# Optimization experiments

Hardware: AMD Instinct MI355X
Metric: run time of the kernel (lower is better)

## Reference

```python
import jax, jax.numpy as jnp
import numpy as np

TAU = 2.0   # membrane time constant
V_TH = 0.5  # firing threshold

@jax.custom_vjp
def spike_fn(v):
    return jnp.where(v > 0, 1.0, 0.0)

def _spike_fwd(v):
    return spike_fn(v), v

def _spike_bwd(v, g):
    # atan surrogate gradient (alpha=2): d s / d v = 1 / (1 + (pi*v)^2)
    sg = 1.0 / (1.0 + (jnp.pi * v) ** 2)
    return (g * sg,)

spike_fn.defvjp(_spike_fwd, _spike_bwd)


def setup_inputs() -> dict:
    key = jax.random.key(0)
    # [batch, neurons, time] -- time on axis 2, matching moveaxis(x, 2, 0)
    x = jax.random.normal(key, (32, 16384, 100), dtype=jnp.float32)
    return {"x": x}


def reference(x):
    x_seq = jnp.moveaxis(x, 2, 0)  # [T, B, N]
    decay = 1.0 - 1.0 / TAU

    def scan_fn(v, x_t):
        v = v * decay + x_t            # leaky integrate
        s = spike_fn(v - V_TH)         # fire
        v = v - s * V_TH               # soft reset
        return v, s

    v_init = jnp.zeros_like(x_seq[0])
    _, spikes = jax.lax.scan(scan_fn, v_init, x_seq)
    return jnp.moveaxis(spikes, 0, 2)  # [B, N, T]
```

## Files before the change

### kernel.cpp

```cpp
#include <hip/hip_runtime.h>
#include <stdint.h>


#define T_STEPS 100
#define T_VEC   25
#define ROWS    64
#define DECAY   0.5f
#define VTH     0.5f

typedef float vfloat4 __attribute__((ext_vector_type(4)));

__device__ __forceinline__ void gll16(const vfloat4* g, vfloat4* l) {
    __builtin_amdgcn_global_load_lds(
        (const __attribute__((address_space(1))) void*)g,
        (__attribute__((address_space(3))) void*)l,
        16, 0, 0);
}

__global__ __launch_bounds__(64) void lif_gll(const float* __restrict__ x,
                                              float* __restrict__ out,
                                              int n_rows) {
    __shared__ vfloat4 tile[ROWS * T_VEC];
    __shared__ uint4   bits[ROWS];

    const int lane = threadIdx.x;
    const int row0 = blockIdx.x * ROWS;
    const int gf0  = row0 * T_VEC;
    const int total_f4 = n_rows * T_VEC;

    const vfloat4* __restrict__ xb = reinterpret_cast<const vfloat4*>(x);

    unsigned int pk0 = 0, pk1 = 0, pk2 = 0, pk3 = 0;

    if (gf0 + ROWS * T_VEC <= total_f4) {
        #pragma unroll
        for (int k = 0; k < T_VEC; ++k)
            gll16(xb + (gf0 + k * 64 + lane), &tile[k * 64]);

        asm volatile("s_waitcnt vmcnt(0)" ::: "memory");
        __builtin_amdgcn_sched_barrier(0);

        float v = 0.0f;
        #pragma unroll
        for (int c = 0; c < T_VEC; ++c) {
            vfloat4 xs = tile[lane * T_VEC + c];
            #pragma unroll
            for (int k = 0; k < 4; ++k) {
                v = v * DECAY + xs[k];
                bool sp = (v - VTH > 0.0f);
                v -= sp ? VTH : 0.0f;
                unsigned int bit = sp ? 1u : 0u;
                const int b = c * 4 + k;
                if      (b < 32) pk0 |= bit << b;
                else if (b < 64) pk1 |= bit << (b - 32);
                else if (b < 96) pk2 |= bit << (b - 64);
                else             pk3 |= bit << (b - 96);
            }
        }
    } else {
        if (row0 + lane < n_rows) {
            const vfloat4* __restrict__ xr =
                xb + (long long)(row0 + lane) * T_VEC;
            float v = 0.0f;
            #pragma unroll
            for (int c = 0; c < T_VEC; ++c) {
                vfloat4 xs = xr[c];
                #pragma unroll
                for (int k = 0; k < 4; ++k) {
                    v = v * DECAY + xs[k];
                    bool sp = (v - VTH > 0.0f);
                    v -= sp ? VTH : 0.0f;
                    unsigned int bit = sp ? 1u : 0u;
                    const int b = c * 4 + k;
                    if      (b < 32) pk0 |= bit << b;
                    else if (b < 64) pk1 |= bit << (b - 32);
                    else if (b < 96) pk2 |= bit << (b - 64);
                    else             pk3 |= bit << (b - 96);
                }
            }
        }
    }

    {
        uint4 w; w.x = pk0; w.y = pk1; w.z = pk2; w.w = pk3;
        bits[lane] = w;
    }
    __syncthreads();

    vfloat4* __restrict__ ob = reinterpret_cast<vfloat4*>(out);
    const unsigned int* bw = reinterpret_cast<const unsigned int*>(bits);
    #pragma unroll
    for (int i = 0; i < T_VEC; ++i) {
        int f = i * 64 + lane;
        int g = gf0 + f;
        if (g < total_f4) {
            int r  = f / T_VEC;
            int c4 = f % T_VEC;
            unsigned int word = bw[r * 4 + (c4 >> 3)];
            unsigned int nib = (word >> ((c4 & 7) * 4)) & 0xFu;
            vfloat4 s;
            s.x = (nib & 1u) ? 1.0f : 0.0f;
            s.y = (nib & 2u) ? 1.0f : 0.0f;
            s.z = (nib & 4u) ? 1.0f : 0.0f;
            s.w = (nib & 8u) ? 1.0f : 0.0f;
            ob[g] = s;
        }
    }
}

extern "C" void kernel_launch(void* const* d_in, const int* in_sizes, int n_in,
                              void* d_out, int out_size, void* d_ws, size_t ws_size,
                              hipStream_t stream) {
    const float* x = (const float*)d_in[0];
    float* out = (float*)d_out;

    int n_rows = in_sizes[0] / T_STEPS;
    int grid = (n_rows + ROWS - 1) / ROWS;

    lif_gll<<<grid, ROWS, 0, stream>>>(x, out, n_rows);
}
```

Measured before the change: 84.72 us.

## Switch to persistent grid with double-buffered async LDS loads of 32-row tiles

Replaces the one-block-per-64-rows kernel with a persistent grid of 1536 blocks. Each block walks 32-row tiles and double-buffers direct global-to-LDS loads, waiting with partial vmcnt counts so the next tile's loads overlap the current tile's scan and stores. This is meant to hide load latency that the old kernel exposed by waiting on all loads before computing. In exchange only half the lanes run the serial scan, tail rows beyond a multiple of 32 are dropped, and there is no barrier between the bits write and the bits reads that the other lanes make.

Result: slower. 100.6 us (+18.7%).

```diff
diff --git a/kernel.cpp b/kernel.cpp
--- a/kernel.cpp
+++ b/kernel.cpp
@@ -1,10 +1,14 @@
 #include <hip/hip_runtime.h>
-#include <stdint.h>
 
 
 #define T_STEPS 100
 #define T_VEC   25
-#define ROWS    64
+#define TROWS   32
+#define TF4     (TROWS * T_VEC)
+#define TPAD    832
+#define NDMA    13
+#define NST     13
+#define GRID    1536
 #define DECAY   0.5f
 #define VTH     0.5f
 
@@ -13,58 +17,60 @@
 __device__ __forceinline__ void gll16(const vfloat4* g, vfloat4* l) {
     __builtin_amdgcn_global_load_lds(
         (const __attribute__((address_space(1))) void*)g,
-        (__attribute__((address_space(3))) void*)l,
-        16, 0, 0);
+        (__attribute__((address_space(3))) void*)l, 16, 0, 0);
 }
 
-__global__ __launch_bounds__(64) void lif_gll(const float* __restrict__ x,
-                                              float* __restrict__ out,
-                                              int n_rows) {
-    __shared__ vfloat4 tile[ROWS * T_VEC];
-    __shared__ uint4   bits[ROWS];
+__global__ __launch_bounds__(64) void lif_pipe_dma(const float* __restrict__ x,
+                                                   float* __restrict__ out,
+                                                   int n_rows) {
+    __shared__ vfloat4 buf[2][TPAD];
+    __shared__ uint4   bits[TROWS];
 
     const int lane = threadIdx.x;
-    const int row0 = blockIdx.x * ROWS;
-    const int gf0  = row0 * T_VEC;
+    const int ntiles = n_rows / TROWS;
     const int total_f4 = n_rows * T_VEC;
+    const vfloat4* __restrict__ xb = reinterpret_cast<const vfloat4*>(x);
+    vfloat4* __restrict__ ob       = reinterpret_cast<vfloat4*>(out);
 
-    const vfloat4* __restrict__ xb = reinterpret_cast<const vfloat4*>(x);
+    int t = blockIdx.x;
+    if (t >= ntiles) return;
 
-    unsigned int pk0 = 0, pk1 = 0, pk2 = 0, pk3 = 0;
+    {
+        int gf0 = t * TF4;
+        #pragma unroll
+        for (int k = 0; k < NDMA; ++k) {
+            int g = gf0 + k * 64 + lane;
+            if (g < total_f4) gll16(xb + g, &buf[0][k * 64]);
+        }
+    }
+    if (t + GRID < ntiles) {
+        int gf0 = (t + GRID) * TF4;
+        #pragma unroll
+        for (int k = 0; k < NDMA; ++k) {
+            int g = gf0 + k * 64 + lane;
+            if (g < total_f4) gll16(xb + g, &buf[1][k * 64]);
+        }
+    }
 
-    if (gf0 + ROWS * T_VEC <= total_f4) {
-        #pragma unroll
-        for (int k = 0; k < T_VEC; ++k)
-            gll16(xb + (gf0 + k * 64 + lane), &tile[k * 64]);
+    int iter = 0;
+    for (; t < ntiles; t += GRID, ++iter) {
+        const int p = iter & 1;
+        const int tn = t + GRID;
 
-        asm volatile("s_waitcnt vmcnt(0)" ::: "memory");
+        {
+            int wn = (iter > 0 ? 13 : 0) + (tn < ntiles ? 13 : 0);
+            if (wn == 26)      asm volatile("s_waitcnt vmcnt(26)" ::: "memory");
+            else if (wn == 13) asm volatile("s_waitcnt vmcnt(13)" ::: "memory");
+            else               asm volatile("s_waitcnt vmcnt(0)"  ::: "memory");
+        }
         __builtin_amdgcn_sched_barrier(0);
 
-        float v = 0.0f;
-        #pragma unroll
-        for (int c = 0; c < T_VEC; ++c) {
-            vfloat4 xs = tile[lane * T_VEC + c];
-            #pragma unroll
-            for (int k = 0; k < 4; ++k) {
-                v = v * DECAY + xs[k];
-                bool sp = (v - VTH > 0.0f);
-                v -= sp ? VTH : 0.0f;
-                unsigned int bit = sp ? 1u : 0u;
-                const int b = c * 4 + k;
-                if      (b < 32) pk0 |= bit << b;
-                else if (b < 64) pk1 |= bit << (b - 32);
-                else if (b < 96) pk2 |= bit << (b - 64);
-                else             pk3 |= bit << (b - 96);
-            }
-        }
-    } else {
-        if (row0 + lane < n_rows) {
-            const vfloat4* __restrict__ xr =
-                xb + (long long)(row0 + lane) * T_VEC;
+        if (lane < TROWS) {
+            unsigned int pk0 = 0, pk1 = 0, pk2 = 0, pk3 = 0;
             float v = 0.0f;
             #pragma unroll
             for (int c = 0; c < T_VEC; ++c) {
-                vfloat4 xs = xr[c];
+                vfloat4 xs = buf[p][lane * T_VEC + c];
                 #pragma unroll
                 for (int k = 0; k < 4; ++k) {
                     v = v * DECAY + xs[k];
@@ -78,33 +84,42 @@
                     else             pk3 |= bit << (b - 96);
                 }
             }
+            uint4 w; w.x = pk0; w.y = pk1; w.z = pk2; w.w = pk3;
+            bits[lane] = w;
         }
-    }
+        __builtin_amdgcn_sched_barrier(0);
 
-    {
-        uint4 w; w.x = pk0; w.y = pk1; w.z = pk2; w.w = pk3;
-        bits[lane] = w;
-    }
-    __syncthreads();
+        {
+            const unsigned int* bw = reinterpret_cast<const unsigned int*>(bits);
+            int gf0 = t * TF4;
+            #pragma unroll
+            for (int i = 0; i < NST; ++i) {
+                int f = i * 64 + lane;
+                if (f < TF4) {
+                    int r  = f / T_VEC;
+                    int c4 = f % T_VEC;
+                    unsigned int word = bw[r * 4 + (c4 >> 3)];
+                    unsigned int nib = (word >> ((c4 & 7) * 4)) & 0xFu;
+                    vfloat4 s;
+                    s.x = (nib & 1u) ? 1.0f : 0.0f;
+                    s.y = (nib & 2u) ? 1.0f : 0.0f;
+                    s.z = (nib & 4u) ? 1.0f : 0.0f;
+                    s.w = (nib & 8u) ? 1.0f : 0.0f;
+                    ob[gf0 + f] = s;
+                }
+            }
+        }
+        __builtin_amdgcn_sched_barrier(0);
 
-    vfloat4* __restrict__ ob = reinterpret_cast<vfloat4*>(out);
-    const unsigned int* bw = reinterpret_cast<const unsigned int*>(bits);
-    #pragma unroll
-    for (int i = 0; i < T_VEC; ++i) {
-        int f = i * 64 + lane;
-        int g = gf0 + f;
-        if (g < total_f4) {
-            int r  = f / T_VEC;
-            int c4 = f % T_VEC;
-            unsigned int word = bw[r * 4 + (c4 >> 3)];
-            unsigned int nib = (word >> ((c4 & 7) * 4)) & 0xFu;
-            vfloat4 s;
-            s.x = (nib & 1u) ? 1.0f : 0.0f;
-            s.y = (nib & 2u) ? 1.0f : 0.0f;
-            s.z = (nib & 4u) ? 1.0f : 0.0f;
-            s.w = (nib & 8u) ? 1.0f : 0.0f;
-            ob[g] = s;
+        if (t + 2 * GRID < ntiles) {
+            int gf0 = (t + 2 * GRID) * TF4;
+            #pragma unroll
+            for (int k = 0; k < NDMA; ++k) {
+                int g = gf0 + k * 64 + lane;
+                if (g < total_f4) gll16(xb + g, &buf[p][k * 64]);
+            }
         }
+        __builtin_amdgcn_sched_barrier(0);
     }
 }
 
@@ -115,7 +130,8 @@
     float* out = (float*)d_out;
 
     int n_rows = in_sizes[0] / T_STEPS;
-    int grid = (n_rows + ROWS - 1) / ROWS;
+    int ntiles = n_rows / TROWS;
+    int grid = (ntiles < GRID) ? ntiles : GRID;
 
-    lif_gll<<<grid, ROWS, 0, stream>>>(x, out, n_rows);
+    lif_pipe_dma<<<grid, 64, 0, stream>>>(x, out, n_rows);
 }
```
